# Kernel optimization log

Measured on AMD Instinct MI355X. Metric: run time of the kernel, lower is better.

The kernel has to match this reference:

```python
import jax, jax.numpy as jnp
import numpy as np

B, T, C, H = 2, 2048, 1024, 16
HID = 4096
EPS = 1e-5
NEG_INF = float('-inf')


def layer_norm(x, w, b):
    mu = jnp.mean(x, axis=-1, keepdims=True)
    var = jnp.mean((x - mu) ** 2, axis=-1, keepdims=True)
    return (x - mu) / jnp.sqrt(var + EPS) * w + b


def setup_inputs() -> dict:
    key = jax.random.key(0)
    ks = jax.random.split(key, 12)
    s = lambda fan_in: 1.0 / np.sqrt(fan_in)
    return {
        'x': jax.random.normal(ks[0], (B, T, C), dtype=jnp.float32),
        'mask': jax.random.randint(ks[1], (B, T), 0, 2) > 0,
        'attn_w': jax.random.normal(ks[2], (C, 3 * C), dtype=jnp.float32) * s(C),
        'attn_b': jnp.zeros((3 * C,), dtype=jnp.float32),
        'proj_w': jax.random.normal(ks[3], (C, C), dtype=jnp.float32) * s(C),
        'proj_b': jnp.zeros((C,), dtype=jnp.float32),
        'ln1_w': jnp.ones((C,), dtype=jnp.float32),
        'ln1_b': jnp.zeros((C,), dtype=jnp.float32),
        'lin1_w': jax.random.normal(ks[4], (C, HID), dtype=jnp.float32) * s(C),
        'lin1_b': jnp.zeros((HID,), dtype=jnp.float32),
        'lin2_w': jax.random.normal(ks[5], (HID, C), dtype=jnp.float32) * s(HID),
        'lin2_b': jnp.zeros((C,), dtype=jnp.float32),
        'ln2_w': jnp.ones((C,), dtype=jnp.float32),
        'ln2_b': jnp.zeros((C,), dtype=jnp.float32),
    }


def reference(x, mask, attn_w, attn_b, proj_w, proj_b, ln1_w, ln1_b,
              lin1_w, lin1_b, lin2_w, lin2_b, ln2_w, ln2_b):
    D = C // H
    # fused QKV projection
    qkv = x @ attn_w + attn_b                      # [B,T,3C]
    q, k, v = jnp.split(qkv, 3, axis=-1)
    q = q.reshape(B, T, H, D).transpose(0, 2, 1, 3)  # [B,H,T,D]
    k = k.reshape(B, T, H, D).transpose(0, 2, 1, 3)
    v = v.reshape(B, T, H, D).transpose(0, 2, 1, 3)
    scale = 1.0 / jnp.sqrt(jnp.asarray(D, dtype=q.dtype))
    scores = jnp.einsum('bhqd,bhkd->bhqk', q, k) * scale  # [B,H,T,T]
    # bidirectional padding mask with forced-true first key column
    m2d = mask[:, None, :] & mask[:, :, None]       # [B,T,T]
    m2d = m2d.at[:, :, 0].set(True)
    bias = jnp.where(m2d, 0.0, NEG_INF).astype(scores.dtype)
    scores = scores + bias[:, None, :, :]
    w = jax.nn.softmax(scores, axis=-1)
    w = jnp.nan_to_num(w, nan=0.0, posinf=0.0, neginf=0.0)
    y = jnp.einsum('bhqk,bhkd->bhqd', w, v)
    y = y.transpose(0, 2, 1, 3).reshape(B, T, C)
    y = y @ proj_w + proj_b
    # residual + post-LN, then MLP + residual + post-LN
    h = layer_norm(x + y, ln1_w, ln1_b)
    ff = jax.nn.gelu(h @ lin1_w + lin1_b, approximate=False) @ lin2_w + lin2_b
    return layer_norm(h + ff, ln2_w, ln2_b)
```

## Files before the change

### kernel.cpp

```cpp
#include <hip/hip_runtime.h>
#include <hip/hip_bf16.h>
#include <math.h>

typedef __attribute__((ext_vector_type(4))) float f32x4;
typedef __attribute__((ext_vector_type(8))) __bf16 bf16x8v;
typedef __attribute__((ext_vector_type(4))) __bf16 bf16x4v;
typedef __attribute__((ext_vector_type(4))) short s16x4;
typedef __attribute__((ext_vector_type(4))) unsigned short u16x4;

#define AS1(p) ((const __attribute__((address_space(1))) void*)(p))
#define AS3(p) ((__attribute__((address_space(3))) void*)(p))

__device__ __forceinline__ unsigned short f2bf(float f) {
  union { float f; unsigned int u; } v; v.f = f;
  unsigned int u = v.u;
  return (unsigned short)((u + 0x7fffu + ((u >> 16) & 1u)) >> 16);
}

__device__ __forceinline__ f32x4 mfma32(bf16x8v a, bf16x8v b, f32x4 c) {
  return __builtin_amdgcn_mfma_f32_16x16x32_bf16(a, b, c, 0, 0, 0);
}

__device__ __forceinline__ f32x4 mfma16(s16x4 a, s16x4 b, f32x4 c) {
#if __has_builtin(__builtin_amdgcn_mfma_f32_16x16x16bf16_1k)
  return __builtin_amdgcn_mfma_f32_16x16x16bf16_1k(a, b, c, 0, 0, 0);
#elif __has_builtin(__builtin_amdgcn_mfma_f32_16x16x16_bf16)
  bf16x4v av, bv;
  __builtin_memcpy(&av, &a, 8);
  __builtin_memcpy(&bv, &b, 8);
  return __builtin_amdgcn_mfma_f32_16x16x16_bf16(av, bv, c, 0, 0, 0);
#else
  asm volatile("v_mfma_f32_16x16x16_bf16 %0, %1, %2, %0\n\ts_nop 7\n\ts_nop 7\n\ts_nop 7"
               : "+v"(c) : "v"(a), "v"(b));
  return c;
#endif
}

__device__ __forceinline__ void async_copy16(const void* g, void* l) {
  __builtin_amdgcn_global_load_lds(AS1(g), AS3(l), 16, 0, 0);
}

__global__ __launch_bounds__(256) void cvt_bf16_kernel(const float* __restrict__ in,
                                                       unsigned short* __restrict__ out, int n4) {
  int i = blockIdx.x * 256 + threadIdx.x;
  if (i < n4) {
    f32x4 v = ((const f32x4*)in)[i];
    u16x4 o;
    o.x = f2bf(v.x); o.y = f2bf(v.y); o.z = f2bf(v.z); o.w = f2bf(v.w);
    ((u16x4*)out)[i] = o;
  }
}

__global__ __launch_bounds__(256) void wtrans_kernel(const float* __restrict__ W,
                                                     unsigned short* __restrict__ Wt,
                                                     int Kd, int Nd) {
  __shared__ float t[32][33];
  int tx = threadIdx.x & 31, ty = threadIdx.x >> 5;
  int bx = blockIdx.x, by = blockIdx.y;
  for (int i = 0; i < 4; ++i) {
    int r = by * 32 + ty + i * 8, c = bx * 32 + tx;
    t[ty + i * 8][tx] = W[(size_t)r * Nd + c];
  }
  __syncthreads();
  for (int i = 0; i < 4; ++i) {
    int nn = bx * 32 + ty + i * 8, kk = by * 32 + tx;
    Wt[(size_t)nn * Kd + kk] = f2bf(t[tx][ty + i * 8]);
  }
}

template <int EPI>
__global__ __launch_bounds__(256) void gemm_bt(const unsigned short* __restrict__ A,
                                               const unsigned short* __restrict__ Bt,
                                               const float* __restrict__ bias,
                                               void* __restrict__ out,
                                               int M, int N, int Kd) {
  __shared__ __align__(16) unsigned short As[128 * 32];
  __shared__ __align__(16) unsigned short Bs[128 * 32];
  int tid = threadIdx.x, wid = tid >> 6, lane = tid & 63;
  int lo = lane & 15, hi = lane >> 4;
  int m0 = blockIdx.y * 128, n0 = blockIdx.x * 128;
  int wm = wid >> 1, wn = wid & 1;
  f32x4 acc[4][4];
  for (int m = 0; m < 4; ++m)
    for (int n = 0; n < 4; ++n) acc[m][n] = f32x4{0.f, 0.f, 0.f, 0.f};
  int sr = lane >> 2;
  int sc = (lane & 3) * 8;
  int nkt = Kd >> 5;
  for (int kt = 0; kt < nkt; ++kt) {
    int k0 = kt * 32;
    for (int i = 0; i < 2; ++i) {
      int ch = wid * 2 + i;
      const unsigned short* ga = A + ((size_t)(m0 + ch * 16 + sr)) * Kd + k0 + sc;
      async_copy16(ga, &As[ch * 512]);
      const unsigned short* gb = Bt + ((size_t)(n0 + ch * 16 + sr)) * Kd + k0 + sc;
      async_copy16(gb, &Bs[ch * 512]);
    }
    __syncthreads();
    bf16x8v af[4], bf_[4];
    for (int m = 0; m < 4; ++m)
      af[m] = *(const bf16x8v*)&As[(wm * 64 + m * 16 + lo) * 32 + hi * 8];
    for (int n = 0; n < 4; ++n)
      bf_[n] = *(const bf16x8v*)&Bs[(wn * 64 + n * 16 + lo) * 32 + hi * 8];
    for (int m = 0; m < 4; ++m)
      for (int n = 0; n < 4; ++n)
        acc[m][n] = mfma32(af[m], bf_[n], acc[m][n]);
    __syncthreads();
  }
  for (int n = 0; n < 4; ++n) {
    int col = n0 + wn * 64 + n * 16 + lo;
    float bv = bias ? bias[col] : 0.f;
    for (int m = 0; m < 4; ++m) {
      int row0 = m0 + wm * 64 + m * 16 + hi * 4;
      for (int j = 0; j < 4; ++j) {
        float v = acc[m][n][j] + bv;
        size_t idx = (size_t)(row0 + j) * N + col;
        if (EPI == 0) {
          ((unsigned short*)out)[idx] = f2bf(v);
        } else if (EPI == 1) {
          ((float*)out)[idx] = v;
        } else {
          float g = 0.5f * v * (1.f + erff(v * 0.70710678118654752f));
          ((unsigned short*)out)[idx] = f2bf(g);
        }
      }
    }
  }
}

__global__ __launch_bounds__(256) void reshape_qk_kernel(const unsigned short* __restrict__ qkv,
                                                         unsigned short* __restrict__ Q,
                                                         unsigned short* __restrict__ K) {
  int idx = blockIdx.x * 256 + threadIdx.x;
  int row = idx >> 9;
  int g = idx & 511;
  int col = g * 4;
  int sec = col >> 10;
  int cc = col & 1023;
  int h = cc >> 6, d = cc & 63;
  int b = row >> 11, t = row & 2047;
  u16x4 v = *(const u16x4*)&qkv[(size_t)row * 3072 + col];
  unsigned short* dst = sec ? K : Q;
  *(u16x4*)&dst[(((size_t)(b * 16 + h)) * 2048 + t) * 64 + d] = v;
}

__global__ __launch_bounds__(256) void vtrans_kernel(const unsigned short* __restrict__ qkv,
                                                     unsigned short* __restrict__ Vt) {
  __shared__ unsigned short t[32][33];
  int tx = threadIdx.x & 31, ty = threadIdx.x >> 5;
  int bx = blockIdx.x, dt = blockIdx.y, bh = blockIdx.z;
  int b = bh >> 4, h = bh & 15;
  for (int i = 0; i < 4; ++i) {
    int trow = bx * 32 + ty + i * 8;
    t[ty + i * 8][tx] = qkv[((size_t)(b * 2048 + trow)) * 3072 + 2048 + h * 64 + dt * 32 + tx];
  }
  __syncthreads();
  for (int i = 0; i < 4; ++i) {
    int d = dt * 32 + ty + i * 8;
    int trow = bx * 32 + tx;
    Vt[((size_t)bh * 64 + d) * 2048 + trow] = t[tx][ty + i * 8];
  }
}

__global__ __launch_bounds__(256) void attn_kernel(const unsigned short* __restrict__ Q,
                                                   const unsigned short* __restrict__ Kt,
                                                   const unsigned short* __restrict__ Vt,
                                                   const int* __restrict__ mask,
                                                   unsigned short* __restrict__ Y) {
  __shared__ __align__(16) unsigned short Kl[2][4096];
  __shared__ __align__(16) unsigned short Vl[2][4096];
  __shared__ float sbias[2048];

  int qt = blockIdx.x, bh = blockIdx.y;
  int b = bh >> 4, h = bh & 15;
  int tid = threadIdx.x, wv = tid >> 6, lane = tid & 63;
  int lo = lane & 15, hi = lane >> 4;

  for (int k = tid; k < 2048; k += 256) {
    int mk = mask[b * 2048 + k];
    sbias[k] = (mk != 0 || k == 0) ? 0.f : -1e30f;
  }

  int r8 = lane >> 3;
  int jsrc = (((lane & 7) ^ r8) << 4);
  const size_t kvbase = (size_t)bh * 2048;

  auto stage = [&](int buf, int kt2) {
    int kbase = kt2 * 64;
#pragma unroll
    for (int i = 0; i < 2; ++i) {
      int r = i * 32 + wv * 8 + r8;
      const unsigned short* gk = Kt + (kvbase + kbase + r) * 64 + (jsrc >> 1);
      async_copy16(gk, (char*)Kl + buf * 8192 + i * 4096 + wv * 1024);
      const unsigned short* gv = Vt + ((size_t)bh * 64 + r) * 2048 + kbase + (jsrc >> 1);
      async_copy16(gv, (char*)Vl + buf * 8192 + i * 4096 + wv * 1024);
    }
  };

  int qrow = qt * 64 + wv * 16 + lo;
  size_t qoff = (kvbase + qrow) * 64;
  bf16x8v Qf0 = *(const bf16x8v*)(Q + qoff + hi * 8);
  bf16x8v Qf1 = *(const bf16x8v*)(Q + qoff + 32 + hi * 8);
  int mq = mask[b * 2048 + qrow];

  float m_run = -1e30f, l_run = 0.f;
  f32x4 acc[4];
#pragma unroll
  for (int c = 0; c < 4; ++c) acc[c] = f32x4{0.f, 0.f, 0.f, 0.f};

  stage(0, 0);
  __syncthreads();

  int sw = (lo & 7) << 4;
  for (int kt = 0; kt < 32; ++kt) {
    int cur = kt & 1;
    if (kt < 31) stage(cur ^ 1, kt + 1);
    int kbase = kt * 64;

    f32x4 s4[4];
#pragma unroll
    for (int kb = 0; kb < 4; ++kb) {
      const char* kr = (const char*)Kl + cur * 8192 + (kb * 16 + lo) * 128;
      bf16x8v K0 = *(const bf16x8v*)(kr + ((hi * 16) ^ sw));
      bf16x8v K1 = *(const bf16x8v*)(kr + ((64 + hi * 16) ^ sw));
      f32x4 z = f32x4{0.f, 0.f, 0.f, 0.f};
      z = mfma32(K0, Qf0, z);
      z = mfma32(K1, Qf1, z);
      s4[kb] = z;
    }

    float p[16], tm = -1e30f;
#pragma unroll
    for (int kb = 0; kb < 4; ++kb) {
      f32x4 bb = *(const f32x4*)&sbias[kbase + kb * 16 + hi * 4];
#pragma unroll
      for (int r = 0; r < 4; ++r) {
        int key = kbase + kb * 16 + hi * 4 + r;
        float sc = s4[kb][r] * 0.125f;
        sc += mq ? bb[r] : (key == 0 ? 0.f : -1e30f);
        p[kb * 4 + r] = sc;
        tm = fmaxf(tm, sc);
      }
    }
    tm = fmaxf(tm, __shfl_xor(tm, 16));
    tm = fmaxf(tm, __shfl_xor(tm, 32));
    float m_new = fmaxf(m_run, tm);
    float fac = __expf(m_run - m_new);
    float ts = 0.f;
#pragma unroll
    for (int i = 0; i < 16; ++i) { p[i] = __expf(p[i] - m_new); ts += p[i]; }
    ts += __shfl_xor(ts, 16);
    ts += __shfl_xor(ts, 32);
    l_run = l_run * fac + ts;
    m_run = m_new;
#pragma unroll
    for (int c = 0; c < 4; ++c) acc[c] *= fac;

    union { unsigned short u[4]; s16x4 s4v; } pk[4];
#pragma unroll
    for (int kb = 0; kb < 4; ++kb)
#pragma unroll
      for (int r = 0; r < 4; ++r) pk[kb].u[r] = f2bf(p[kb * 4 + r]);

#pragma unroll
    for (int c = 0; c < 4; ++c) {
      const char* vr = (const char*)Vl + cur * 8192 + (c * 16 + lo) * 128;
#pragma unroll
      for (int kk = 0; kk < 4; ++kk) {
        s16x4 V0 = *(const s16x4*)(vr + ((kk * 32 + hi * 8) ^ sw));
        acc[c] = mfma16(V0, pk[kk].s4v, acc[c]);
      }
    }
    __syncthreads();
  }

  float invl = 1.f / l_run;
  size_t yrow = ((size_t)(b * 2048 + qrow)) * 1024 + h * 64;
#pragma unroll
  for (int c = 0; c < 4; ++c)
#pragma unroll
    for (int r = 0; r < 4; ++r)
      Y[yrow + c * 16 + hi * 4 + r] = f2bf(acc[c][r] * invl);
}

__global__ __launch_bounds__(256) void ln_kernel(const float* __restrict__ A,
                                                 const float* __restrict__ Bsrc,
                                                 const float* __restrict__ w,
                                                 const float* __restrict__ bias,
                                                 float* __restrict__ outF,
                                                 unsigned short* __restrict__ outB) {
  int row = blockIdx.x, tid = threadIdx.x;
  f32x4 r = ((const f32x4*)A)[row * 256 + tid] + ((const f32x4*)Bsrc)[row * 256 + tid];
  float s = r.x + r.y + r.z + r.w;
  float q = r.x * r.x + r.y * r.y + r.z * r.z + r.w * r.w;
  for (int off = 1; off < 64; off <<= 1) {
    s += __shfl_xor(s, off);
    q += __shfl_xor(q, off);
  }
  __shared__ float ls[4], lq[4];
  int wid = tid >> 6, lane = tid & 63;
  if (lane == 0) { ls[wid] = s; lq[wid] = q; }
  __syncthreads();
  s = ls[0] + ls[1] + ls[2] + ls[3];
  q = lq[0] + lq[1] + lq[2] + lq[3];
  float mu = s * (1.f / 1024.f);
  float var = q * (1.f / 1024.f) - mu * mu;
  float rstd = rsqrtf(var + 1e-5f);
  f32x4 wv = ((const f32x4*)w)[tid];
  f32x4 bv = ((const f32x4*)bias)[tid];
  f32x4 o = (r - mu) * rstd * wv + bv;
  if (outF) ((f32x4*)outF)[row * 256 + tid] = o;
  if (outB) {
    u16x4 ob;
    ob.x = f2bf(o.x); ob.y = f2bf(o.y); ob.z = f2bf(o.z); ob.w = f2bf(o.w);
    ((u16x4*)outB)[row * 256 + tid] = ob;
  }
}

extern "C" void kernel_launch(void* const* d_in, const int* in_sizes, int n_in,
                              void* d_out, int out_size, void* d_ws, size_t ws_size,
                              hipStream_t stream) {
  const float* x      = (const float*)d_in[0];
  const int*   mask   = (const int*)d_in[1];
  const float* attn_w = (const float*)d_in[2];
  const float* attn_b = (const float*)d_in[3];
  const float* proj_w = (const float*)d_in[4];
  const float* proj_b = (const float*)d_in[5];
  const float* ln1_w  = (const float*)d_in[6];
  const float* ln1_b  = (const float*)d_in[7];
  const float* lin1_w = (const float*)d_in[8];
  const float* lin1_b = (const float*)d_in[9];
  const float* lin2_w = (const float*)d_in[10];
  const float* lin2_b = (const float*)d_in[11];
  const float* ln2_w  = (const float*)d_in[12];
  const float* ln2_b  = (const float*)d_in[13];
  float* out = (float*)d_out;

  char* ws = (char*)d_ws;
  size_t off = 0;
  auto alloc = [&](size_t bytes) { char* p = ws + off; off += (bytes + 255) & ~(size_t)255; return p; };

  unsigned short* attn_wT = (unsigned short*)alloc((size_t)3072 * 1024 * 2);
  unsigned short* proj_wT = (unsigned short*)alloc((size_t)1024 * 1024 * 2);
  unsigned short* lin1_wT = (unsigned short*)alloc((size_t)4096 * 1024 * 2);
  unsigned short* lin2_wT = (unsigned short*)alloc((size_t)1024 * 4096 * 2);
  char* regionA = alloc((size_t)3 * 8388608);
  char* regionB = alloc((size_t)8388608);
  char* regionC = alloc((size_t)25165824);
  float* h_f32  = (float*)alloc((size_t)4096 * 1024 * 4);
  unsigned short* h_bf16 = (unsigned short*)alloc((size_t)4096 * 1024 * 2);
  float* mlp2   = (float*)alloc((size_t)4096 * 1024 * 4);

  unsigned short* Qb  = (unsigned short*)regionA;
  unsigned short* Kb  = (unsigned short*)(regionA + 8388608);
  unsigned short* Vtb = (unsigned short*)(regionA + 16777216);
  unsigned short* ff1 = (unsigned short*)regionA;
  unsigned short* xb  = (unsigned short*)regionB;
  unsigned short* qkv = (unsigned short*)regionC;
  unsigned short* Yb  = (unsigned short*)regionC;
  float* proj_out     = (float*)(regionC + 8388608);

  wtrans_kernel<<<dim3(96, 32), 256, 0, stream>>>(attn_w, attn_wT, 1024, 3072);
  wtrans_kernel<<<dim3(32, 32), 256, 0, stream>>>(proj_w, proj_wT, 1024, 1024);
  wtrans_kernel<<<dim3(128, 32), 256, 0, stream>>>(lin1_w, lin1_wT, 1024, 4096);
  wtrans_kernel<<<dim3(32, 128), 256, 0, stream>>>(lin2_w, lin2_wT, 4096, 1024);
  cvt_bf16_kernel<<<4096, 256, 0, stream>>>(x, xb, 4096 * 1024 / 4);

  gemm_bt<0><<<dim3(24, 32), 256, 0, stream>>>(xb, attn_wT, attn_b, qkv, 4096, 3072, 1024);
  reshape_qk_kernel<<<8192, 256, 0, stream>>>(qkv, Qb, Kb);
  vtrans_kernel<<<dim3(64, 2, 32), 256, 0, stream>>>(qkv, Vtb);

  attn_kernel<<<dim3(32, 32), 256, 0, stream>>>(Qb, Kb, Vtb, mask, Yb);

  gemm_bt<1><<<dim3(8, 32), 256, 0, stream>>>(Yb, proj_wT, proj_b, proj_out, 4096, 1024, 1024);
  ln_kernel<<<4096, 256, 0, stream>>>(x, proj_out, ln1_w, ln1_b, h_f32, h_bf16);

  gemm_bt<2><<<dim3(32, 32), 256, 0, stream>>>(h_bf16, lin1_wT, lin1_b, ff1, 4096, 4096, 1024);
  gemm_bt<1><<<dim3(8, 32), 256, 0, stream>>>(ff1, lin2_wT, lin2_b, mlp2, 4096, 1024, 4096);
  ln_kernel<<<4096, 256, 0, stream>>>(h_f32, mlp2, ln2_w, ln2_b, out, nullptr);
}
```

Measured before the change: 471.8 us.

## Double-buffer GEMM, swizzle blocks, fuse QKV scatter, lazy softmax rescale

The GEMM gains double-buffered LDS staging so the next K tile loads while MFMAs run. It also gains an XCD-aware 1D block swizzle. The QKV GEMM now writes Q, K and transposed V directly from its epilogue, which removes the reshape and V-transpose kernels and the intermediate qkv buffer. The attention kernel switches to exp2 with a folded log2e scale and only rescales the running max when it grows by more than a threshold. The risks are scattered strided stores in the V epilogue and doubled LDS use, which may lower occupancy.

Result: faster. 456.7 us (-3.2%).

```diff
diff --git a/kernel.cpp b/kernel.cpp
--- a/kernel.cpp
+++ b/kernel.cpp
@@ -73,12 +73,20 @@
                                                const unsigned short* __restrict__ Bt,
                                                const float* __restrict__ bias,
                                                void* __restrict__ out,
-                                               int M, int N, int Kd) {
-  __shared__ __align__(16) unsigned short As[128 * 32];
-  __shared__ __align__(16) unsigned short Bs[128 * 32];
+                                               unsigned short* __restrict__ outQ,
+                                               unsigned short* __restrict__ outK,
+                                               unsigned short* __restrict__ outV,
+                                               int M, int N, int Kd, int gx) {
+  __shared__ __align__(16) unsigned short As[2][128 * 32];
+  __shared__ __align__(16) unsigned short Bs[2][128 * 32];
   int tid = threadIdx.x, wid = tid >> 6, lane = tid & 63;
   int lo = lane & 15, hi = lane >> 4;
-  int m0 = blockIdx.y * 128, n0 = blockIdx.x * 128;
+
+  int wg = blockIdx.x, nwg = gridDim.x;
+  int cpx = nwg >> 3;
+  int swz = (wg & 7) * cpx + (wg >> 3);
+  int m0 = (swz / gx) * 128, n0 = (swz % gx) * 128;
+
   int wm = wid >> 1, wn = wid & 1;
   f32x4 acc[4][4];
   for (int m = 0; m < 4; ++m)
@@ -86,78 +94,71 @@
   int sr = lane >> 2;
   int sc = (lane & 3) * 8;
   int nkt = Kd >> 5;
-  for (int kt = 0; kt < nkt; ++kt) {
+
+  auto stage = [&](int buf, int kt) {
     int k0 = kt * 32;
+#pragma unroll
     for (int i = 0; i < 2; ++i) {
       int ch = wid * 2 + i;
       const unsigned short* ga = A + ((size_t)(m0 + ch * 16 + sr)) * Kd + k0 + sc;
-      async_copy16(ga, &As[ch * 512]);
+      async_copy16(ga, &As[buf][ch * 512]);
       const unsigned short* gb = Bt + ((size_t)(n0 + ch * 16 + sr)) * Kd + k0 + sc;
-      async_copy16(gb, &Bs[ch * 512]);
-    }
-    __syncthreads();
+      async_copy16(gb, &Bs[buf][ch * 512]);
+    }
+  };
+
+  stage(0, 0);
+  __syncthreads();
+  for (int kt = 0; kt < nkt; ++kt) {
+    int cur = kt & 1;
+    if (kt + 1 < nkt) stage(cur ^ 1, kt + 1);
     bf16x8v af[4], bf_[4];
+#pragma unroll
     for (int m = 0; m < 4; ++m)
-      af[m] = *(const bf16x8v*)&As[(wm * 64 + m * 16 + lo) * 32 + hi * 8];
+      af[m] = *(const bf16x8v*)&As[cur][(wm * 64 + m * 16 + lo) * 32 + hi * 8];
+#pragma unroll
     for (int n = 0; n < 4; ++n)
-      bf_[n] = *(const bf16x8v*)&Bs[(wn * 64 + n * 16 + lo) * 32 + hi * 8];
+      bf_[n] = *(const bf16x8v*)&Bs[cur][(wn * 64 + n * 16 + lo) * 32 + hi * 8];
+#pragma unroll
     for (int m = 0; m < 4; ++m)
+#pragma unroll
       for (int n = 0; n < 4; ++n)
         acc[m][n] = mfma32(af[m], bf_[n], acc[m][n]);
     __syncthreads();
   }
+
+#pragma unroll
   for (int n = 0; n < 4; ++n) {
     int col = n0 + wn * 64 + n * 16 + lo;
     float bv = bias ? bias[col] : 0.f;
+#pragma unroll
     for (int m = 0; m < 4; ++m) {
       int row0 = m0 + wm * 64 + m * 16 + hi * 4;
+#pragma unroll
       for (int j = 0; j < 4; ++j) {
         float v = acc[m][n][j] + bv;
-        size_t idx = (size_t)(row0 + j) * N + col;
+        int row = row0 + j;
+        size_t idx = (size_t)row * N + col;
         if (EPI == 0) {
           ((unsigned short*)out)[idx] = f2bf(v);
         } else if (EPI == 1) {
           ((float*)out)[idx] = v;
-        } else {
+        } else if (EPI == 2) {
           float g = 0.5f * v * (1.f + erff(v * 0.70710678118654752f));
           ((unsigned short*)out)[idx] = f2bf(g);
+        } else {
+          int c2 = col & 1023, h = c2 >> 6, d = c2 & 63;
+          int bq = row >> 11, t = row & 2047;
+          unsigned short val = f2bf(v);
+          if (col < 2048) {
+            unsigned short* dst = (col < 1024) ? outQ : outK;
+            dst[(((size_t)(bq * 16 + h)) * 2048 + t) * 64 + d] = val;
+          } else {
+            outV[(((size_t)(bq * 16 + h)) * 64 + d) * 2048 + t] = val;
+          }
         }
       }
     }
-  }
-}
-
-__global__ __launch_bounds__(256) void reshape_qk_kernel(const unsigned short* __restrict__ qkv,
-                                                         unsigned short* __restrict__ Q,
-                                                         unsigned short* __restrict__ K) {
-  int idx = blockIdx.x * 256 + threadIdx.x;
-  int row = idx >> 9;
-  int g = idx & 511;
-  int col = g * 4;
-  int sec = col >> 10;
-  int cc = col & 1023;
-  int h = cc >> 6, d = cc & 63;
-  int b = row >> 11, t = row & 2047;
-  u16x4 v = *(const u16x4*)&qkv[(size_t)row * 3072 + col];
-  unsigned short* dst = sec ? K : Q;
-  *(u16x4*)&dst[(((size_t)(b * 16 + h)) * 2048 + t) * 64 + d] = v;
-}
-
-__global__ __launch_bounds__(256) void vtrans_kernel(const unsigned short* __restrict__ qkv,
-                                                     unsigned short* __restrict__ Vt) {
-  __shared__ unsigned short t[32][33];
-  int tx = threadIdx.x & 31, ty = threadIdx.x >> 5;
-  int bx = blockIdx.x, dt = blockIdx.y, bh = blockIdx.z;
-  int b = bh >> 4, h = bh & 15;
-  for (int i = 0; i < 4; ++i) {
-    int trow = bx * 32 + ty + i * 8;
-    t[ty + i * 8][tx] = qkv[((size_t)(b * 2048 + trow)) * 3072 + 2048 + h * 64 + dt * 32 + tx];
-  }
-  __syncthreads();
-  for (int i = 0; i < 4; ++i) {
-    int d = dt * 32 + ty + i * 8;
-    int trow = bx * 32 + tx;
-    Vt[((size_t)bh * 64 + d) * 2048 + trow] = t[tx][ty + i * 8];
   }
 }
 
@@ -202,6 +203,7 @@
   bf16x8v Qf1 = *(const bf16x8v*)(Q + qoff + 32 + hi * 8);
   int mq = mask[b * 2048 + qrow];
 
+  const float scale2 = 0.125f * 1.44269504088896340736f;
   float m_run = -1e30f, l_run = 0.f;
   f32x4 acc[4];
 #pragma unroll
@@ -235,7 +237,7 @@
 #pragma unroll
       for (int r = 0; r < 4; ++r) {
         int key = kbase + kb * 16 + hi * 4 + r;
-        float sc = s4[kb][r] * 0.125f;
+        float sc = s4[kb][r] * scale2;
         sc += mq ? bb[r] : (key == 0 ? 0.f : -1e30f);
         p[kb * 4 + r] = sc;
         tm = fmaxf(tm, sc);
@@ -243,17 +245,20 @@
     }
     tm = fmaxf(tm, __shfl_xor(tm, 16));
     tm = fmaxf(tm, __shfl_xor(tm, 32));
-    float m_new = fmaxf(m_run, tm);
-    float fac = __expf(m_run - m_new);
+    if (__any(tm > m_run + 8.0f)) {
+      float m_new = fmaxf(m_run, tm);
+      float fac = exp2f(m_run - m_new);
+      l_run *= fac;
+#pragma unroll
+      for (int c = 0; c < 4; ++c) acc[c] *= fac;
+      m_run = m_new;
+    }
     float ts = 0.f;
 #pragma unroll
-    for (int i = 0; i < 16; ++i) { p[i] = __expf(p[i] - m_new); ts += p[i]; }
+    for (int i = 0; i < 16; ++i) { p[i] = exp2f(p[i] - m_run); ts += p[i]; }
     ts += __shfl_xor(ts, 16);
     ts += __shfl_xor(ts, 32);
-    l_run = l_run * fac + ts;
-    m_run = m_new;
-#pragma unroll
-    for (int c = 0; c < 4; ++c) acc[c] *= fac;
+    l_run += ts;
 
     union { unsigned short u[4]; s16x4 s4v; } pk[4];
 #pragma unroll
@@ -355,7 +360,6 @@
   unsigned short* Vtb = (unsigned short*)(regionA + 16777216);
   unsigned short* ff1 = (unsigned short*)regionA;
   unsigned short* xb  = (unsigned short*)regionB;
-  unsigned short* qkv = (unsigned short*)regionC;
   unsigned short* Yb  = (unsigned short*)regionC;
   float* proj_out     = (float*)(regionC + 8388608);
 
@@ -365,16 +369,18 @@
   wtrans_kernel<<<dim3(32, 128), 256, 0, stream>>>(lin2_w, lin2_wT, 4096, 1024);
   cvt_bf16_kernel<<<4096, 256, 0, stream>>>(x, xb, 4096 * 1024 / 4);
 
-  gemm_bt<0><<<dim3(24, 32), 256, 0, stream>>>(xb, attn_wT, attn_b, qkv, 4096, 3072, 1024);
-  reshape_qk_kernel<<<8192, 256, 0, stream>>>(qkv, Qb, Kb);
-  vtrans_kernel<<<dim3(64, 2, 32), 256, 0, stream>>>(qkv, Vtb);
+  gemm_bt<3><<<768, 256, 0, stream>>>(xb, attn_wT, attn_b, nullptr, Qb, Kb, Vtb,
+                                      4096, 3072, 1024, 24);
 
   attn_kernel<<<dim3(32, 32), 256, 0, stream>>>(Qb, Kb, Vtb, mask, Yb);
 
-  gemm_bt<1><<<dim3(8, 32), 256, 0, stream>>>(Yb, proj_wT, proj_b, proj_out, 4096, 1024, 1024);
+  gemm_bt<1><<<256, 256, 0, stream>>>(Yb, proj_wT, proj_b, proj_out, nullptr, nullptr, nullptr,
+                                      4096, 1024, 1024, 8);
   ln_kernel<<<4096, 256, 0, stream>>>(x, proj_out, ln1_w, ln1_b, h_f32, h_bf16);
 
-  gemm_bt<2><<<dim3(32, 32), 256, 0, stream>>>(h_bf16, lin1_wT, lin1_b, ff1, 4096, 4096, 1024);
-  gemm_bt<1><<<dim3(8, 32), 256, 0, stream>>>(ff1, lin2_wT, lin2_b, mlp2, 4096, 1024, 4096);
+  gemm_bt<2><<<1024, 256, 0, stream>>>(h_bf16, lin1_wT, lin1_b, ff1, nullptr, nullptr, nullptr,
+                                       4096, 4096, 1024, 32);
+  gemm_bt<1><<<256, 256, 0, stream>>>(ff1, lin2_wT, lin2_b, mlp2, nullptr, nullptr, nullptr,
+                                      4096, 1024, 4096, 8);
   ln_kernel<<<4096, 256, 0, stream>>>(h_f32, mlp2, ln2_w, ln2_b, out, nullptr);
 }
```
